# Optimization experiments

Measured on AMD Instinct MI355X. Metric: run time of the kernel, lower is better.

## Reference

```python
import jax, jax.numpy as jnp
import numpy as np

B, N, D = 512, 500000, 128
K = 100


def setup_inputs() -> dict:
    key = jax.random.key(0)
    kq, kc = jax.random.split(key)
    queries = jax.random.normal(kq, (B, D), dtype=jnp.float32)
    candidates = jax.random.normal(kc, (N, D), dtype=jnp.float32)
    identifiers = jnp.arange(N, dtype=jnp.int32)
    return {
        "queries": queries,
        "candidates": candidates,
        "identifiers": identifiers,
        "num_candidates": K,
    }


def reference(queries, candidates, identifiers, num_candidates):
    # scores: [B, N] dense similarity matrix (dot product)
    scores = jnp.einsum("bd,nd->bn", queries, candidates)
    # top-k per query row
    values, indices = jax.lax.top_k(scores, num_candidates)  # [B, K] each
    top_ids = jnp.take(identifiers, indices, axis=0)          # [B, K]
    return values, top_ids
```

## Files before the change

kernel.cpp:

```cpp
#include <hip/hip_runtime.h>
#include <cfloat>


#define D_DIM 128
#define K_TOP 100
#define THRESH_SIGMA 3.25f
#define CAP_MAX 512
#define KEEP_MAXF 256

typedef short bf16x8 __attribute__((ext_vector_type(8)));
typedef float f32x4 __attribute__((ext_vector_type(4)));

__device__ __forceinline__ unsigned short f2bf(float x) {
    unsigned u = __float_as_uint(x);
    return (unsigned short)((u + 0x7FFFu + ((u >> 16) & 1u)) >> 16);
}

__device__ __forceinline__ unsigned long long make_key(float v, unsigned id) {
    unsigned vb = __float_as_uint(v);
    unsigned vm = (vb & 0x80000000u) ? ~vb : (vb | 0x80000000u);
    return ((unsigned long long)vm << 32) | (0xFFFFFFFFu - id);
}

template <int S>
__device__ inline void bitonic_sort_u64(unsigned long long* buf) {
    for (int k = 2; k <= S; k <<= 1) {
        for (int j = k >> 1; j > 0; j >>= 1) {
            __syncthreads();
            for (int i = threadIdx.x; i < S; i += blockDim.x) {
                int l = i ^ j;
                if (l > i) {
                    unsigned long long a = buf[i], b = buf[l];
                    bool sw = ((i & k) == 0) ? (a > b) : (a < b);
                    if (sw) { buf[i] = b; buf[l] = a; }
                }
            }
        }
    }
    __syncthreads();
}

__global__ void prep2_kernel(const float* __restrict__ Qm, float* __restrict__ thr,
                             int* __restrict__ cnt, int B) {
    int b = blockIdx.x * blockDim.x + threadIdx.x;
    if (b >= B) return;
    float s = 0.f;
    for (int d = 0; d < D_DIM; ++d) { float v = Qm[(size_t)b * D_DIM + d]; s = fmaf(v, v, s); }
    thr[b] = THRESH_SIGMA * sqrtf(s);
    cnt[b] = 0;
}

__global__ void qfrag_kernel(const float* __restrict__ Qm, uint4* __restrict__ qf,
                             int B, int nch) {
    int tid = blockIdx.x * blockDim.x + threadIdx.x;
    int total = nch * 8 * 4 * 64;
    if (tid >= total) return;
    int l  = tid & 63;
    int ks = (tid >> 6) & 3;
    int qb = (tid >> 8) & 7;
    int qch = tid >> 11;
    int qrow = qch * 128 + qb * 16 + (l & 15);
    int k0 = ks * 32 + (l >> 4) * 8;
    uint4 o = make_uint4(0u, 0u, 0u, 0u);
    if (qrow < B) {
        const float* src = Qm + (size_t)qrow * D_DIM + k0;
        unsigned r[4];
#pragma unroll
        for (int j = 0; j < 4; ++j)
            r[j] = (unsigned)f2bf(src[2 * j]) | ((unsigned)f2bf(src[2 * j + 1]) << 16);
        o = make_uint4(r[0], r[1], r[2], r[3]);
    }
    qf[tid] = o;
}

__global__ __launch_bounds__(256, 2) void mfma_filter_kernel(
    const float* __restrict__ cand, const bf16x8* __restrict__ qfrag,
    const float* __restrict__ thr, unsigned* __restrict__ idbuf,
    int* __restrict__ cnt, int N, int B, int cap, int nch) {
    __shared__ char cl[32768];
    const int t = threadIdx.x;
    const int w = t >> 6;
    const int l = t & 63;
    const int c0 = blockIdx.x * 128;

#pragma unroll
    for (int i = 0; i < 16; ++i) {
        int f4 = i * 256 + t;
        int row = f4 >> 5;
        int colf4 = f4 & 31;
        int gc = c0 + row;
        float4 v = make_float4(0.f, 0.f, 0.f, 0.f);
        if (gc < N) v = *reinterpret_cast<const float4*>(cand + (size_t)gc * D_DIM + colf4 * 4);
        uint2 pk;
        pk.x = (unsigned)f2bf(v.x) | ((unsigned)f2bf(v.y) << 16);
        pk.y = (unsigned)f2bf(v.z) | ((unsigned)f2bf(v.w) << 16);
        int byte = row * 256 + ((colf4 * 8) ^ ((row & 7) << 4));
        *reinterpret_cast<uint2*>(cl + byte) = pk;
    }
    __syncthreads();

#pragma unroll 1
    for (int qch = w; qch < nch; qch += 4) {
        bf16x8 bq[8][4];
#pragma unroll
        for (int qb = 0; qb < 8; ++qb)
#pragma unroll
            for (int ks = 0; ks < 4; ++ks)
                bq[qb][ks] = qfrag[((qch * 8 + qb) * 4 + ks) * 64 + l];

        float tvq[8];
#pragma unroll
        for (int qb = 0; qb < 8; ++qb) {
            int qg = qch * 128 + qb * 16 + (l & 15);
            tvq[qb] = (qg < B) ? thr[qg] : 3.0e38f;
        }

#pragma unroll
        for (int cb = 0; cb < 8; ++cb) {
            int row = cb * 16 + (l & 15);
            int sw = (row & 7) << 4;
            bf16x8 af[4];
#pragma unroll
            for (int ks = 0; ks < 4; ++ks) {
                int byte = row * 256 + ((ks * 64 + ((l >> 4) * 16)) ^ sw);
                af[ks] = *reinterpret_cast<const bf16x8*>(cl + byte);
            }

            f32x4 acc[8];
#pragma unroll
            for (int qb = 0; qb < 8; ++qb) acc[qb] = (f32x4){0.f, 0.f, 0.f, 0.f};
#pragma unroll
            for (int ks = 0; ks < 4; ++ks) {
                bf16x8 a = af[ks];
#pragma unroll
                for (int qb = 0; qb < 8; ++qb)
                    acc[qb] = __builtin_amdgcn_mfma_f32_16x16x32_bf16(
                        a, bq[qb][ks], acc[qb], 0, 0, 0);
            }

#pragma unroll
            for (int qb = 0; qb < 8; ++qb) {
                float tv = tvq[qb];
                f32x4 a = acc[qb];
                float m = fmaxf(fmaxf(a[0], a[1]), fmaxf(a[2], a[3]));
                if (m > tv) {
                    int qg = qch * 128 + qb * 16 + (l & 15);
#pragma unroll
                    for (int r = 0; r < 4; ++r) {
                        if (a[r] > tv) {
                            int cid = c0 + cb * 16 + ((l >> 4) << 2) + r;
                            if (cid < N) {
                                int pos = atomicAdd(&cnt[qg], 1);
                                if (pos < cap) idbuf[(size_t)qg * cap + pos] = (unsigned)cid;
                            }
                        }
                    }
                }
            }
        }
    }
}

__global__ void fallback_kernel(const float* __restrict__ Qm, const float* __restrict__ cand,
                                unsigned* __restrict__ idbuf, int* __restrict__ cnt,
                                int N, int cap) {
    int q = blockIdx.x;
    int c0 = cnt[q];
    if (c0 >= K_TOP && c0 <= cap) return;
    int keep = (cap < KEEP_MAXF) ? cap : KEEP_MAXF;

    __shared__ unsigned long long buf[2048];
    __shared__ float qrow[D_DIM];
    __shared__ int bn;
    __shared__ float theta;
    __shared__ int validn;
    for (int i = threadIdx.x; i < D_DIM; i += blockDim.x) qrow[i] = Qm[(size_t)q * D_DIM + i];
    for (int i = threadIdx.x; i < 2048; i += blockDim.x) buf[i] = 0ULL;
    if (threadIdx.x == 0) { bn = 0; theta = -3.0e38f; }
    __syncthreads();

    for (int base = 0; base < N; base += blockDim.x) {
        int c = base + threadIdx.x;
        if (c < N) {
            float s = 0.f;
            for (int d = 0; d < D_DIM; ++d) s = fmaf(qrow[d], cand[(size_t)c * D_DIM + d], s);
            if (s > theta) {
                int p = atomicAdd(&bn, 1);
                if (p < 2048) buf[p] = make_key(s, (unsigned)c);
            }
        }
        __syncthreads();
        if (bn > 2048 - 256 - 8) {
            bitonic_sort_u64<2048>(buf);
            unsigned long long kv = (threadIdx.x < (unsigned)keep) ? buf[2047 - threadIdx.x] : 0ULL;
            __syncthreads();
            for (int i = threadIdx.x; i < 2048; i += blockDim.x) buf[i] = 0ULL;
            __syncthreads();
            if (threadIdx.x < (unsigned)keep) buf[threadIdx.x] = kv;
            if ((int)threadIdx.x == keep - 1) {
                unsigned vm = (unsigned)(kv >> 32);
                unsigned vb = (vm & 0x80000000u) ? (vm ^ 0x80000000u) : ~vm;
                theta = __uint_as_float(vb) - 0.01f;
            }
            if (threadIdx.x == 0) bn = keep;
            __syncthreads();
        }
    }
    bitonic_sort_u64<2048>(buf);
    if (threadIdx.x == 0) validn = 0;
    __syncthreads();
    unsigned long long kv = (threadIdx.x < (unsigned)keep) ? buf[2047 - threadIdx.x] : 0ULL;
    if (kv != 0ULL) atomicAdd(&validn, 1);
    __syncthreads();
    if ((int)threadIdx.x < validn && threadIdx.x < (unsigned)keep) {
        unsigned id = 0xFFFFFFFFu - (unsigned)(kv & 0xFFFFFFFFu);
        if (id < (unsigned)N) idbuf[(size_t)q * cap + threadIdx.x] = id;
    }
    if (threadIdx.x == 0) cnt[q] = (validn < keep) ? validn : keep;
}

__device__ __forceinline__ float np_lane_chain(float q0, float b0v, float q1, float b1v,
                                               float q2, float b2v, float q3, float b3v,
                                               float acc) {
    float t = __fadd_rn(__fmul_rn(q3, b3v), acc);
    t = __fadd_rn(__fmul_rn(q2, b2v), t);
    t = __fadd_rn(__fmul_rn(q1, b1v), t);
    return __fadd_rn(__fmul_rn(q0, b0v), t);
}

__device__ __forceinline__ float np_score(const float* __restrict__ qrow,
                                          const float* __restrict__ crow) {
    float acc0 = 0.f, acc1 = 0.f, acc2 = 0.f, acc3 = 0.f;
#pragma unroll
    for (int d0 = 0; d0 < D_DIM; d0 += 16) {
        float4 b0 = *reinterpret_cast<const float4*>(crow + d0 + 0);
        float4 b1 = *reinterpret_cast<const float4*>(crow + d0 + 4);
        float4 b2 = *reinterpret_cast<const float4*>(crow + d0 + 8);
        float4 b3 = *reinterpret_cast<const float4*>(crow + d0 + 12);
        acc0 = np_lane_chain(qrow[d0 + 0], b0.x, qrow[d0 + 4], b1.x,
                             qrow[d0 + 8], b2.x, qrow[d0 + 12], b3.x, acc0);
        acc1 = np_lane_chain(qrow[d0 + 1], b0.y, qrow[d0 + 5], b1.y,
                             qrow[d0 + 9], b2.y, qrow[d0 + 13], b3.y, acc1);
        acc2 = np_lane_chain(qrow[d0 + 2], b0.z, qrow[d0 + 6], b1.z,
                             qrow[d0 + 10], b2.z, qrow[d0 + 14], b3.z, acc2);
        acc3 = np_lane_chain(qrow[d0 + 3], b0.w, qrow[d0 + 7], b1.w,
                             qrow[d0 + 11], b2.w, qrow[d0 + 15], b3.w, acc3);
    }
    return __fadd_rn(__fadd_rn(acc0, acc1), __fadd_rn(acc2, acc3));
}

__global__ __launch_bounds__(256) void select_kernel(
    const float* __restrict__ Qm, const float* __restrict__ cand,
    const unsigned* __restrict__ idbuf, const int* __restrict__ cnt,
    const int* __restrict__ ident, float* __restrict__ out, int N, int B, int cap) {
    __shared__ unsigned long long skey[CAP_MAX];
    __shared__ float qrow[D_DIM];
    int q = blockIdx.x;
    for (int i = threadIdx.x; i < D_DIM; i += blockDim.x) qrow[i] = Qm[(size_t)q * D_DIM + i];
    __syncthreads();

    int n = cnt[q]; if (n > cap) n = cap; if (n > CAP_MAX) n = CAP_MAX;
    for (int i = threadIdx.x; i < CAP_MAX; i += blockDim.x) {
        unsigned long long key = 0ULL;
        if (i < n) {
            unsigned id = idbuf[(size_t)q * cap + i];
            if (id < (unsigned)N) {
                float s = np_score(qrow, cand + (size_t)id * D_DIM);
                key = make_key(s, id);
            }
        }
        skey[i] = key;
    }

    bitonic_sort_u64<CAP_MAX>(skey);

    for (int t = threadIdx.x; t < K_TOP; t += blockDim.x) {
        unsigned long long key = skey[CAP_MAX - 1 - t];
        unsigned vm = (unsigned)(key >> 32);
        unsigned vb = (vm & 0x80000000u) ? (vm ^ 0x80000000u) : ~vm;
        unsigned id = 0xFFFFFFFFu - (unsigned)(key & 0xFFFFFFFFu);
        if (id >= (unsigned)N) id = 0;
        out[(size_t)q * K_TOP + t] = __uint_as_float(vb);
        out[(size_t)B * K_TOP + (size_t)q * K_TOP + t] = (float)ident[id];
    }
}

extern "C" void kernel_launch(void* const* d_in, const int* in_sizes, int n_in,
                              void* d_out, int out_size, void* d_ws, size_t ws_size,
                              hipStream_t stream) {
    const float* queries = (const float*)d_in[0];
    const float* cands   = (const float*)d_in[1];
    const int*   ident   = (const int*)d_in[2];
    const int B = in_sizes[0] / D_DIM;
    const int N = in_sizes[2];
    float* out = (float*)d_out;
    const int nch = (B + 127) >> 7;

    char* ws = (char*)d_ws;
    int*   cnt = (int*)ws;
    float* thr = (float*)(ws + 2048);
    uint4* qfrag = (uint4*)(ws + 4096);
    size_t ids_off = 4096 + (size_t)nch * 32768;
    unsigned* idbuf = (unsigned*)(ws + ids_off);
    int cap = CAP_MAX;
    if (ws_size > ids_off) {
        size_t fit = (ws_size - ids_off) / ((size_t)B * 4);
        if (fit < (size_t)cap) cap = (int)fit;
    } else cap = 1;
    if (cap < 1) cap = 1;

    prep2_kernel<<<(B + 255) / 256, 256, 0, stream>>>(queries, thr, cnt, B);
    int qft = nch * 2048;
    qfrag_kernel<<<(qft + 255) / 256, 256, 0, stream>>>(queries, qfrag, B, nch);

    int gx = (N + 127) / 128;
    mfma_filter_kernel<<<gx, 256, 0, stream>>>(
        cands, (const bf16x8*)qfrag, thr, idbuf, cnt, N, B, cap, nch);

    fallback_kernel<<<B, 256, 0, stream>>>(queries, cands, idbuf, cnt, N, cap);

    select_kernel<<<B, 256, 0, stream>>>(queries, cands, idbuf, cnt, ident, out, N, B, cap);
}
```

Baseline: 203.7 us.

## Make MFMA filter persistent with double-buffered candidate tiles and resident query fragments

The filter kernel becomes a persistent grid of 512 blocks that stride over candidate tiles. Each wave loads its query fragments and thresholds once. Candidate tiles are double-buffered in shared memory, so global loads for the next tile are issued in halves while the current tile is being computed. The goal is to hide global-load latency and remove per-tile query-fragment reloads. The cost is twice the LDS per block, extra registers for staging, and fixed-grid load balance; batches larger than 512 queries are split into several launches.

New measurement: 290.6 us. +42.7%, slower.

```diff
diff --git a/kernel.cpp b/kernel.cpp
--- a/kernel.cpp
+++ b/kernel.cpp
@@ -7,6 +7,7 @@
 #define THRESH_SIGMA 3.25f
 #define CAP_MAX 512
 #define KEEP_MAXF 256
+#define FGRID 512
 
 typedef short bf16x8 __attribute__((ext_vector_type(8)));
 typedef float f32x4 __attribute__((ext_vector_type(4)));
@@ -76,56 +77,66 @@
 __global__ __launch_bounds__(256, 2) void mfma_filter_kernel(
     const float* __restrict__ cand, const bf16x8* __restrict__ qfrag,
     const float* __restrict__ thr, unsigned* __restrict__ idbuf,
-    int* __restrict__ cnt, int N, int B, int cap, int nch) {
-    __shared__ char cl[32768];
+    int* __restrict__ cnt, int N, int Bg, int cap, int nch, int ntiles) {
+    __shared__ char cl[2][32768];
     const int t = threadIdx.x;
     const int w = t >> 6;
     const int l = t & 63;
-    const int c0 = blockIdx.x * 128;
-
-#pragma unroll
-    for (int i = 0; i < 16; ++i) {
-        int f4 = i * 256 + t;
-        int row = f4 >> 5;
-        int colf4 = f4 & 31;
-        int gc = c0 + row;
-        float4 v = make_float4(0.f, 0.f, 0.f, 0.f);
-        if (gc < N) v = *reinterpret_cast<const float4*>(cand + (size_t)gc * D_DIM + colf4 * 4);
-        uint2 pk;
-        pk.x = (unsigned)f2bf(v.x) | ((unsigned)f2bf(v.y) << 16);
-        pk.y = (unsigned)f2bf(v.z) | ((unsigned)f2bf(v.w) << 16);
-        int byte = row * 256 + ((colf4 * 8) ^ ((row & 7) << 4));
-        *reinterpret_cast<uint2*>(cl + byte) = pk;
-    }
-    __syncthreads();
-
-#pragma unroll 1
-    for (int qch = w; qch < nch; qch += 4) {
-        bf16x8 bq[8][4];
-#pragma unroll
-        for (int qb = 0; qb < 8; ++qb)
-#pragma unroll
-            for (int ks = 0; ks < 4; ++ks)
-                bq[qb][ks] = qfrag[((qch * 8 + qb) * 4 + ks) * 64 + l];
-
-        float tvq[8];
-#pragma unroll
-        for (int qb = 0; qb < 8; ++qb) {
-            int qg = qch * 128 + qb * 16 + (l & 15);
-            tvq[qb] = (qg < B) ? thr[qg] : 3.0e38f;
-        }
-
-#pragma unroll
-        for (int cb = 0; cb < 8; ++cb) {
+
+    const bool qvalid = (w < nch);
+    const int qch = qvalid ? w : (nch - 1);
+    bf16x8 bq[8][4];
+#pragma unroll
+    for (int qb = 0; qb < 8; ++qb)
+#pragma unroll
+        for (int ks = 0; ks < 4; ++ks)
+            bq[qb][ks] = qfrag[((qch * 8 + qb) * 4 + ks) * 64 + l];
+    float tvq[8];
+#pragma unroll
+    for (int qb = 0; qb < 8; ++qb) {
+        int qg = qch * 128 + qb * 16 + (l & 15);
+        tvq[qb] = (qvalid && qg < Bg) ? thr[qg] : 3.0e38f;
+    }
+
+    float4 ra[8];
+    auto stage_load = [&](int tile, int h) {
+        int c0t = tile * 128;
+#pragma unroll
+        for (int i = 0; i < 8; ++i) {
+            int f4 = (h * 8 + i) * 256 + t;
+            int row = f4 >> 5;
+            int colf4 = f4 & 31;
+            int gc = c0t + row;
+            float4 v = make_float4(0.f, 0.f, 0.f, 0.f);
+            if (gc < N) v = *reinterpret_cast<const float4*>(cand + (size_t)gc * D_DIM + colf4 * 4);
+            ra[i] = v;
+        }
+    };
+    auto stage_write = [&](int buf, int h) {
+#pragma unroll
+        for (int i = 0; i < 8; ++i) {
+            int f4 = (h * 8 + i) * 256 + t;
+            int row = f4 >> 5;
+            int colf4 = f4 & 31;
+            uint2 pk;
+            pk.x = (unsigned)f2bf(ra[i].x) | ((unsigned)f2bf(ra[i].y) << 16);
+            pk.y = (unsigned)f2bf(ra[i].z) | ((unsigned)f2bf(ra[i].w) << 16);
+            int byte = row * 256 + ((colf4 * 8) ^ ((row & 7) << 4));
+            *reinterpret_cast<uint2*>(cl[buf] + byte) = pk;
+        }
+    };
+    auto compute_half = [&](int buf, int h, int c0) {
+#pragma unroll
+        for (int cbi = 0; cbi < 4; ++cbi) {
+            int cb = h * 4 + cbi;
             int row = cb * 16 + (l & 15);
             int sw = (row & 7) << 4;
             bf16x8 af[4];
 #pragma unroll
             for (int ks = 0; ks < 4; ++ks) {
                 int byte = row * 256 + ((ks * 64 + ((l >> 4) * 16)) ^ sw);
-                af[ks] = *reinterpret_cast<const bf16x8*>(cl + byte);
-            }
-
+                af[ks] = *reinterpret_cast<const bf16x8*>(cl[buf] + byte);
+            }
             f32x4 acc[8];
 #pragma unroll
             for (int qb = 0; qb < 8; ++qb) acc[qb] = (f32x4){0.f, 0.f, 0.f, 0.f};
@@ -137,7 +148,6 @@
                     acc[qb] = __builtin_amdgcn_mfma_f32_16x16x32_bf16(
                         a, bq[qb][ks], acc[qb], 0, 0, 0);
             }
-
 #pragma unroll
             for (int qb = 0; qb < 8; ++qb) {
                 float tv = tvq[qb];
@@ -158,6 +168,31 @@
                 }
             }
         }
+    };
+
+    int tile = blockIdx.x;
+    if (tile >= ntiles) return;
+    stage_load(tile, 0); stage_write(0, 0);
+    stage_load(tile, 1); stage_write(0, 1);
+    __syncthreads();
+
+    int cur = 0;
+#pragma unroll 1
+    while (true) {
+        int nxt = tile + FGRID;
+        bool have_next = (nxt < ntiles);
+        int c0 = tile * 128;
+
+        if (have_next) stage_load(nxt, 0);
+        compute_half(cur, 0, c0);
+        if (have_next) stage_write(cur ^ 1, 0);
+        if (have_next) stage_load(nxt, 1);
+        compute_half(cur, 1, c0);
+        if (have_next) stage_write(cur ^ 1, 1);
+
+        if (!have_next) break;
+        __syncthreads();
+        cur ^= 1; tile = nxt;
     }
 }
 
@@ -295,6 +330,7 @@
     const int N = in_sizes[2];
     float* out = (float*)d_out;
     const int nch = (B + 127) >> 7;
+    const int ntiles = (N + 127) / 128;
 
     char* ws = (char*)d_ws;
     int*   cnt = (int*)ws;
@@ -313,9 +349,15 @@
     int qft = nch * 2048;
     qfrag_kernel<<<(qft + 255) / 256, 256, 0, stream>>>(queries, qfrag, B, nch);
 
-    int gx = (N + 127) / 128;
-    mfma_filter_kernel<<<gx, 256, 0, stream>>>(
-        cands, (const bf16x8*)qfrag, thr, idbuf, cnt, N, B, cap, nch);
+    int ngrp = (nch + 3) / 4;
+    for (int g = 0; g < ngrp; ++g) {
+        int nch_g = nch - g * 4; if (nch_g > 4) nch_g = 4;
+        int B_g = B - g * 512; if (B_g > 512) B_g = 512;
+        mfma_filter_kernel<<<FGRID, 256, 0, stream>>>(
+            cands, (const bf16x8*)(qfrag + (size_t)g * 8192),
+            thr + (size_t)g * 512, idbuf + (size_t)g * 512 * cap,
+            cnt + (size_t)g * 512, N, B_g, cap, nch_g, ntiles);
+    }
 
     fallback_kernel<<<B, 256, 0, stream>>>(queries, cands, idbuf, cnt, N, cap);
 
```

## Make filter kernel persistent with double-buffered direct-to-LDS candidate loads

Applied to the files above, without the earlier changes.

The filter kernel now runs as a persistent grid of 512 blocks that loop over 64-row candidate tiles. Each wave keeps one 128-query chunk's fragments and thresholds in registers for the whole kernel. Candidate tiles are loaded straight into LDS as fp32 with global_load_lds and double-buffered, so the next tile's load overlaps the MFMA work on the current one. Conversion to bf16 moves to LDS read time and uses truncation instead of rounding, which slightly changes the scores seen by the threshold filter. Query groups beyond 512 are handled by launching the kernel once per group, and the LDS footprint doubles.

Result: faster. 165.6 us (-18.7%).

```diff
diff --git a/kernel.cpp b/kernel.cpp
--- a/kernel.cpp
+++ b/kernel.cpp
@@ -7,6 +7,8 @@
 #define THRESH_SIGMA 3.25f
 #define CAP_MAX 512
 #define KEEP_MAXF 256
+#define FGRID 512
+#define TROWS 64
 
 typedef short bf16x8 __attribute__((ext_vector_type(8)));
 typedef float f32x4 __attribute__((ext_vector_type(4)));
@@ -76,89 +78,118 @@
 __global__ __launch_bounds__(256, 2) void mfma_filter_kernel(
     const float* __restrict__ cand, const bf16x8* __restrict__ qfrag,
     const float* __restrict__ thr, unsigned* __restrict__ idbuf,
-    int* __restrict__ cnt, int N, int B, int cap, int nch) {
-    __shared__ char cl[32768];
+    int* __restrict__ cnt, int N, int Bg, int cap, int nch, int ntiles) {
+    __shared__ __align__(16) char cl[2][TROWS * 512];
     const int t = threadIdx.x;
     const int w = t >> 6;
     const int l = t & 63;
-    const int c0 = blockIdx.x * 128;
-
-#pragma unroll
-    for (int i = 0; i < 16; ++i) {
-        int f4 = i * 256 + t;
-        int row = f4 >> 5;
-        int colf4 = f4 & 31;
-        int gc = c0 + row;
-        float4 v = make_float4(0.f, 0.f, 0.f, 0.f);
-        if (gc < N) v = *reinterpret_cast<const float4*>(cand + (size_t)gc * D_DIM + colf4 * 4);
-        uint2 pk;
-        pk.x = (unsigned)f2bf(v.x) | ((unsigned)f2bf(v.y) << 16);
-        pk.y = (unsigned)f2bf(v.z) | ((unsigned)f2bf(v.w) << 16);
-        int byte = row * 256 + ((colf4 * 8) ^ ((row & 7) << 4));
-        *reinterpret_cast<uint2*>(cl + byte) = pk;
-    }
-    __syncthreads();
-
+
+    const bool qv = (w < nch);
+    const int qch = qv ? w : (nch > 0 ? nch - 1 : 0);
+    bf16x8 bq[8][4];
+#pragma unroll
+    for (int qb = 0; qb < 8; ++qb)
+#pragma unroll
+        for (int ks = 0; ks < 4; ++ks)
+            bq[qb][ks] = qfrag[((qch * 8 + qb) * 4 + ks) * 64 + l];
+    float tvq[8];
+#pragma unroll
+    for (int qb = 0; qb < 8; ++qb) {
+        int qg = qch * 128 + qb * 16 + (l & 15);
+        tvq[qb] = (qv && qg < Bg) ? thr[qg] : 3.0e38f;
+    }
+
+    int tile = blockIdx.x;
+    if (tile >= ntiles) return;
+
+#define STAGE(BUFI, T)                                                              \
+    do {                                                                            \
+        int c0s = (T) * TROWS;                                                      \
+        _Pragma("unroll")                                                           \
+        for (int i = 0; i < 8; ++i) {                                               \
+            int rl = (w * 8 + i) * 2 + (l >> 5);                                    \
+            int gr = c0s + rl; if (gr > N - 1) gr = N - 1;                          \
+            int ug = (l & 31) ^ (rl & 7);                                           \
+            const float* srcp = cand + (size_t)gr * D_DIM + ug * 4;                 \
+            __builtin_amdgcn_global_load_lds(                                       \
+                (const __attribute__((address_space(1))) void*)srcp,                \
+                (__attribute__((address_space(3))) void*)(&cl[BUFI][(w * 8 + i) * 1024]), \
+                16, 0, 0);                                                          \
+        }                                                                           \
+    } while (0)
+
+    STAGE(0, tile);
+    int cur = 0;
 #pragma unroll 1
-    for (int qch = w; qch < nch; qch += 4) {
-        bf16x8 bq[8][4];
-#pragma unroll
-        for (int qb = 0; qb < 8; ++qb)
-#pragma unroll
-            for (int ks = 0; ks < 4; ++ks)
-                bq[qb][ks] = qfrag[((qch * 8 + qb) * 4 + ks) * 64 + l];
-
-        float tvq[8];
-#pragma unroll
-        for (int qb = 0; qb < 8; ++qb) {
-            int qg = qch * 128 + qb * 16 + (l & 15);
-            tvq[qb] = (qg < B) ? thr[qg] : 3.0e38f;
-        }
-
-#pragma unroll
-        for (int cb = 0; cb < 8; ++cb) {
-            int row = cb * 16 + (l & 15);
-            int sw = (row & 7) << 4;
-            bf16x8 af[4];
-#pragma unroll
-            for (int ks = 0; ks < 4; ++ks) {
-                int byte = row * 256 + ((ks * 64 + ((l >> 4) * 16)) ^ sw);
-                af[ks] = *reinterpret_cast<const bf16x8*>(cl + byte);
-            }
-
-            f32x4 acc[8];
-#pragma unroll
-            for (int qb = 0; qb < 8; ++qb) acc[qb] = (f32x4){0.f, 0.f, 0.f, 0.f};
-#pragma unroll
-            for (int ks = 0; ks < 4; ++ks) {
-                bf16x8 a = af[ks];
-#pragma unroll
-                for (int qb = 0; qb < 8; ++qb)
-                    acc[qb] = __builtin_amdgcn_mfma_f32_16x16x32_bf16(
-                        a, bq[qb][ks], acc[qb], 0, 0, 0);
-            }
-
-#pragma unroll
-            for (int qb = 0; qb < 8; ++qb) {
-                float tv = tvq[qb];
-                f32x4 a = acc[qb];
-                float m = fmaxf(fmaxf(a[0], a[1]), fmaxf(a[2], a[3]));
-                if (m > tv) {
-                    int qg = qch * 128 + qb * 16 + (l & 15);
-#pragma unroll
-                    for (int r = 0; r < 4; ++r) {
-                        if (a[r] > tv) {
-                            int cid = c0 + cb * 16 + ((l >> 4) << 2) + r;
-                            if (cid < N) {
-                                int pos = atomicAdd(&cnt[qg], 1);
-                                if (pos < cap) idbuf[(size_t)qg * cap + pos] = (unsigned)cid;
+    while (true) {
+        int nxt = tile + FGRID;
+        bool hn = (nxt < ntiles);
+        if (hn) {
+            STAGE(cur ^ 1, nxt);
+            asm volatile("s_waitcnt vmcnt(8)" ::: "memory");
+        } else {
+            asm volatile("s_waitcnt vmcnt(0)" ::: "memory");
+        }
+        __builtin_amdgcn_s_barrier();
+
+        {
+            const char* bp = cl[cur];
+            int c0 = tile * TROWS;
+#pragma unroll
+            for (int cb = 0; cb < 4; ++cb) {
+                int r = cb * 16 + (l & 15);
+                int sb = r * 512, s = r & 7;
+                bf16x8 af[4];
+#pragma unroll
+                for (int ks = 0; ks < 4; ++ks) {
+                    int u0 = ks * 8 + (l >> 4) * 2;
+                    f32x4 f0 = *reinterpret_cast<const f32x4*>(bp + sb + ((u0 ^ s) << 4));
+                    f32x4 f1 = *reinterpret_cast<const f32x4*>(bp + sb + (((u0 + 1) ^ s) << 4));
+                    union { bf16x8 v; unsigned u[4]; } p;
+                    p.u[0] = (__float_as_uint(f0[0]) >> 16) | (__float_as_uint(f0[1]) & 0xFFFF0000u);
+                    p.u[1] = (__float_as_uint(f0[2]) >> 16) | (__float_as_uint(f0[3]) & 0xFFFF0000u);
+                    p.u[2] = (__float_as_uint(f1[0]) >> 16) | (__float_as_uint(f1[1]) & 0xFFFF0000u);
+                    p.u[3] = (__float_as_uint(f1[2]) >> 16) | (__float_as_uint(f1[3]) & 0xFFFF0000u);
+                    af[ks] = p.v;
+                }
+                f32x4 acc[8];
+#pragma unroll
+                for (int qb = 0; qb < 8; ++qb) acc[qb] = (f32x4){0.f, 0.f, 0.f, 0.f};
+#pragma unroll
+                for (int ks = 0; ks < 4; ++ks) {
+                    bf16x8 a = af[ks];
+#pragma unroll
+                    for (int qb = 0; qb < 8; ++qb)
+                        acc[qb] = __builtin_amdgcn_mfma_f32_16x16x32_bf16(
+                            a, bq[qb][ks], acc[qb], 0, 0, 0);
+                }
+#pragma unroll
+                for (int qb = 0; qb < 8; ++qb) {
+                    float tv = tvq[qb];
+                    f32x4 a = acc[qb];
+                    float m = fmaxf(fmaxf(a[0], a[1]), fmaxf(a[2], a[3]));
+                    if (m > tv) {
+                        int qg = qch * 128 + qb * 16 + (l & 15);
+#pragma unroll
+                        for (int rr = 0; rr < 4; ++rr) {
+                            if (a[rr] > tv) {
+                                int cid = c0 + cb * 16 + ((l >> 4) << 2) + rr;
+                                if (cid < N) {
+                                    int pos = atomicAdd(&cnt[qg], 1);
+                                    if (pos < cap) idbuf[(size_t)qg * cap + pos] = (unsigned)cid;
+                                }
                             }
                         }
                     }
                 }
             }
         }
-    }
+
+        if (!hn) break;
+        __builtin_amdgcn_s_barrier();
+        cur ^= 1; tile = nxt;
+    }
+#undef STAGE
 }
 
 __global__ void fallback_kernel(const float* __restrict__ Qm, const float* __restrict__ cand,
@@ -295,6 +326,7 @@
     const int N = in_sizes[2];
     float* out = (float*)d_out;
     const int nch = (B + 127) >> 7;
+    const int ntiles = (N + TROWS - 1) / TROWS;
 
     char* ws = (char*)d_ws;
     int*   cnt = (int*)ws;
@@ -313,9 +345,15 @@
     int qft = nch * 2048;
     qfrag_kernel<<<(qft + 255) / 256, 256, 0, stream>>>(queries, qfrag, B, nch);
 
-    int gx = (N + 127) / 128;
-    mfma_filter_kernel<<<gx, 256, 0, stream>>>(
-        cands, (const bf16x8*)qfrag, thr, idbuf, cnt, N, B, cap, nch);
+    int ngrp = (nch + 3) / 4;
+    for (int g = 0; g < ngrp; ++g) {
+        int nch_g = nch - g * 4; if (nch_g > 4) nch_g = 4;
+        int B_g = B - g * 512; if (B_g > 512) B_g = 512;
+        mfma_filter_kernel<<<FGRID, 256, 0, stream>>>(
+            cands, (const bf16x8*)(qfrag + (size_t)g * 8192),
+            thr + (size_t)g * 512, idbuf + (size_t)g * 512 * cap,
+            cnt + (size_t)g * 512, N, B_g, cap, nch_g, ntiles);
+    }
 
     fallback_kernel<<<B, 256, 0, stream>>>(queries, cands, idbuf, cnt, N, cap);
 
```
